# Optimization experiments

Hardware: AMD Instinct MI355X
Metric: run time of the kernel (lower is better)

## Reference

```python
import jax, jax.numpy as jnp
import numpy as np

B, H, S, D = 2, 16, 2048, 64
NUM_BUCKETS = 32
MAX_DISTANCE = 256


def setup_inputs() -> dict:
    key = jax.random.key(0)
    kq, kk, kv, kb, kl = jax.random.split(key, 5)
    q = jax.random.normal(kq, (B, H, S, D), dtype=jnp.float32)
    k = jax.random.normal(kk, (B, H, S, D), dtype=jnp.float32)
    v = jax.random.normal(kv, (B, H, S, D), dtype=jnp.float32)
    bias_table = jax.random.normal(kb, (NUM_BUCKETS, H), dtype=jnp.float32)
    event_length = jax.random.randint(kl, (B,), 1, S + 1, dtype=jnp.int64)
    return {"q": q, "k": k, "v": v, "bias_table": bias_table, "event_length": event_length}


def _relative_position_bucket(relative_position):
    # T5-style bucketing exactly as the torch module: n = -rel_pos
    half = NUM_BUCKETS // 2  # 16
    n = -relative_position
    is_small = n < half
    # guard log for the branch not taken (n<=0); where() masks it out
    nf = jnp.maximum(n, 1).astype(jnp.float32)
    val_if_large = half + jnp.minimum(
        jnp.log(nf / half) / np.log(MAX_DISTANCE / half) * (NUM_BUCKETS - half),
        NUM_BUCKETS - 1 - half,
    ).astype(jnp.int32)
    ret = jnp.where(is_small, n, val_if_large)
    return jnp.clip(ret, 0, NUM_BUCKETS - 1)


def _compute_bias(bias_table, seq_len):
    ctx = jnp.arange(seq_len)[:, None]
    mem = jnp.arange(seq_len)[None, :]
    rp_bucket = _relative_position_bucket(mem - ctx)  # (S,S)
    values = bias_table[rp_bucket]                    # (S,S,H)
    return jnp.transpose(values, (2, 0, 1))[None]     # (1,H,S,S)


def reference(q, k, v, bias_table, event_length):
    seq_len = q.shape[2]
    head_dim = q.shape[3]
    # scaled QK^T: (B,H,S,S)
    logits = jnp.einsum("bhsd,bhtd->bhst", q, k) / np.sqrt(head_dim).astype(np.float32)
    logits = logits + _compute_bias(bias_table, seq_len)
    # key-side padding mask from per-event lengths
    mask = jnp.arange(seq_len)[None, None, None, :] < event_length[:, None, None, None]
    logits = jnp.where(mask, logits, jnp.float32(-1e9))
    attn = jax.nn.softmax(logits, axis=-1)
    # dropout p=0.01 omitted (eval-mode deterministic reference)
    return jnp.einsum("bhst,bhtd->bhsd", attn, v)
```

## Files before the change

kernel.cpp:

```cpp
#include <hip/hip_runtime.h>

#define B_ 2
#define H_ 16
#define S_ 2048
#define D_ 64
#define BQ 128
#define BK 64
#define NQB (S_ / BQ)
#define NKT (S_ / BK)
#define LDSH 64
#define NBUF 3
#define LOG2E 1.4426950408889634f
#define FIXM 10.0f

#if __has_builtin(__builtin_amdgcn_exp2f)
#define EXP2F(x) __builtin_amdgcn_exp2f(x)
#else
#define EXP2F(x) __expf((x) * 0.6931471805599453f)
#endif

typedef _Float16 half8 __attribute__((ext_vector_type(8)));
typedef _Float16 half4 __attribute__((ext_vector_type(4)));
typedef __fp16   fp16x2 __attribute__((ext_vector_type(2)));
typedef float floatx4 __attribute__((ext_vector_type(4)));

#define VT_OFF  24576
#define LUT_OFF 49152
#define OX_STR  66
#define LX_OFF  33792
#define SMEM_BYTES 50176

__global__ __launch_bounds__(512, 4)
void t5_attn_kernel(const float* __restrict__ qg_, const float* __restrict__ kg_,
                    const float* __restrict__ vg_, const float* __restrict__ bt,
                    const int* __restrict__ elen, float* __restrict__ outg_)
{
    __shared__ __align__(16) unsigned char smem[SMEM_BYTES];
    _Float16* KL = reinterpret_cast<_Float16*>(smem);
    _Float16* VT = reinterpret_cast<_Float16*>(smem + VT_OFF);
    float*   lut = reinterpret_cast<float*>(smem + LUT_OFF);

    const int tid  = threadIdx.x;
    const int wave = tid >> 6;
    const int lane = tid & 63;
    const int quad = lane >> 4;
    const int t16  = lane & 15;
    const int t8   = t16 & 7;
    const int wq   = wave >> 1;
    const int kh   = wave & 1;

    const int f    = blockIdx.x + NQB * (blockIdx.y + H_ * blockIdx.z);
    const int qblk = (f >> 3) & 15;
    const int bh   = (f & 7) | ((f >> 7) << 3);
    const int h    = bh & 15;
    const int b    = bh >> 4;

    if (tid < 256) {
        int n = tid;
        int bucket;
        if (n < 16) {
            bucket = n;
        } else {
            int vl = (int)(__log2f((float)n * 0.0625f) * 4.0f);
            bucket = 16 + (vl < 15 ? vl : 15);
        }
        lut[n] = bt[bucket * H_ + h] * LOG2E - FIXM;
    }
    const float sh_next = FIXM - bt[h] * LOG2E;
    const float sh_far  = FIXM - bt[31 * H_ + h] * LOG2E;

    const int len = (elen[1] == 0) ? elen[2 * b] : elen[b];
    const int ntiles = (len + BK - 1) >> 6;

    const size_t bhoff = ((size_t)b * H_ + h) * (size_t)(S_ * D_);
    const float* qptr = qg_ + bhoff;
    const float* kptr = kg_ + bhoff;
    const float* vptr = vg_ + bhoff;
    float*       optr = outg_ + bhoff;

    half8 qf[2][2];
    {
        const float qscale = 0.125f * LOG2E;
        #pragma unroll
        for (int rg = 0; rg < 2; ++rg) {
            const int row = qblk * BQ + wq * 32 + rg * 16 + t16;
            const float* qp = qptr + (size_t)row * D_ + quad * 8;
            #pragma unroll
            for (int c = 0; c < 2; ++c) {
                const float4* pq = reinterpret_cast<const float4*>(qp + c * 32);
                float4 x0 = pq[0], x1 = pq[1];
                half8 hv;
                hv[0] = (_Float16)(x0.x * qscale); hv[1] = (_Float16)(x0.y * qscale);
                hv[2] = (_Float16)(x0.z * qscale); hv[3] = (_Float16)(x0.w * qscale);
                hv[4] = (_Float16)(x1.x * qscale); hv[5] = (_Float16)(x1.y * qscale);
                hv[6] = (_Float16)(x1.z * qscale); hv[7] = (_Float16)(x1.w * qscale);
                qf[rg][c] = hv;
            }
        }
    }

    floatx4 acc[2][4];
    float l_[2];
    #pragma unroll
    for (int rg = 0; rg < 2; ++rg) {
        #pragma unroll
        for (int nb = 0; nb < 4; ++nb) acc[rg][nb] = floatx4{0.f, 0.f, 0.f, 0.f};
        l_[rg] = 0.f;
    }

    const int i_lo = qblk * BQ + wq * 32;

    auto pack4 = [](const floatx4& v) -> half4 {
        fp16x2 lo = __builtin_amdgcn_cvt_pkrtz(v[0], v[1]);
        fp16x2 hi = __builtin_amdgcn_cvt_pkrtz(v[2], v[3]);
        half4 w;
        w[0] = (_Float16)lo[0]; w[1] = (_Float16)lo[1];
        w[2] = (_Float16)hi[0]; w[3] = (_Float16)hi[1];
        return w;
    };

    const int krow = tid >> 3;
    const int kst  = krow * LDSH + (((tid & 7) ^ (krow & 7)) << 3);
    const int vst  = lane * LDSH + ((wave ^ (lane & 7)) << 3);
    const int c8w  = (tid & 7) << 3;

    float4 kx0, kx1;
    float  vx[8];
    auto prefetch = [&](int kt) {
        const int ktc = kt < NKT ? kt : NKT - 1;
        const float4* pp = reinterpret_cast<const float4*>(
            kptr + (size_t)(ktc * BK + krow) * D_ + c8w);
        kx0 = pp[0];
        kx1 = pp[1];
        const float* vb = vptr + (size_t)(ktc * BK + wave * 8) * D_ + lane;
        #pragma unroll
        for (int jj = 0; jj < 8; ++jj)
            vx[jj] = vb[jj * D_];
    };
    auto stage = [&](int bufe) {
        half8 hv;
        hv[0]=(_Float16)kx0.x; hv[1]=(_Float16)kx0.y; hv[2]=(_Float16)kx0.z; hv[3]=(_Float16)kx0.w;
        hv[4]=(_Float16)kx1.x; hv[5]=(_Float16)kx1.y; hv[6]=(_Float16)kx1.z; hv[7]=(_Float16)kx1.w;
        *reinterpret_cast<half8*>(KL + bufe + kst) = hv;
        half8 vv;
        #pragma unroll
        for (int jj = 0; jj < 8; ++jj) vv[jj] = (_Float16)vx[jj];
        *reinterpret_cast<half8*>(VT + bufe + vst) = vv;
    };

    prefetch(0);
    stage(0);
    prefetch(1);
    __syncthreads();

    int cur = 0;
    for (int kt = 0; kt < ntiles; ++kt) {
        const int nxt  = (cur + 1 == NBUF) ? 0 : cur + 1;
        const int curb = cur * 4096;
        const int nxtb = nxt * 4096;

        stage(nxtb);
        prefetch(kt + 2);

        const int keybase = kt * BK + kh * 32;

        const bool unif_next = (i_lo + 31 <= keybase);
        const bool unif_far  = (i_lo >= keybase + 247);
        const float cinit = unif_next ? -sh_next : (unif_far ? -sh_far : 0.f);
        const floatx4 ci = {cinit, cinit, cinit, cinit};

        floatx4 sa[2][2];
        #pragma unroll
        for (int rg = 0; rg < 2; ++rg)
            #pragma unroll
            for (int nb = 0; nb < 2; ++nb) sa[rg][nb] = ci;
        __builtin_amdgcn_s_setprio(1);
        #pragma unroll
        for (int kc = 0; kc < 2; ++kc) {
            #pragma unroll
            for (int nb = 0; nb < 2; ++nb) {
                half8 af = *reinterpret_cast<const half8*>(
                    KL + curb + (kh * 32 + nb * 16 + t16) * LDSH +
                    ((((kc << 2) | quad) ^ t8) << 3));
                sa[0][nb] = __builtin_amdgcn_mfma_f32_16x16x32_f16(af, qf[0][kc], sa[0][nb], 0, 0, 0);
                sa[1][nb] = __builtin_amdgcn_mfma_f32_16x16x32_f16(af, qf[1][kc], sa[1][nb], 0, 0, 0);
            }
        }
        __builtin_amdgcn_s_setprio(0);

        half4 bvv[4][2];
        #pragma unroll
        for (int nb = 0; nb < 4; ++nb) {
            #pragma unroll
            for (int s = 0; s < 2; ++s) {
                bvv[nb][s] = *reinterpret_cast<const half4*>(
                    VT + curb + (nb * 16 + t16) * LDSH +
                    ((((kh << 2) | (s << 1) | (quad >> 1)) ^ t8) << 3) +
                    ((quad & 1) << 2));
            }
        }

        if (!unif_next && !unif_far) {
            #pragma unroll
            for (int rg = 0; rg < 2; ++rg) {
                const int d0 = i_lo + rg * 16 + t16 - keybase - quad * 4;
                #pragma unroll
                for (int nb = 0; nb < 2; ++nb) {
                    #pragma unroll
                    for (int r = 0; r < 4; ++r) {
                        int d = d0 - nb * 16 - r;
                        d = d < 0 ? 0 : (d > 255 ? 255 : d);
                        sa[rg][nb][r] += lut[d];
                    }
                }
            }
        }
        if ((kt == ntiles - 1) && (len & 63)) {
            #pragma unroll
            for (int nb = 0; nb < 2; ++nb) {
                #pragma unroll
                for (int r = 0; r < 4; ++r) {
                    bool valid = (keybase + nb * 16 + quad * 4 + r) < len;
                    #pragma unroll
                    for (int rg = 0; rg < 2; ++rg)
                        sa[rg][nb][r] = valid ? sa[rg][nb][r] : -1e30f;
                }
            }
        }

        #pragma unroll
        for (int rg = 0; rg < 2; ++rg) {
            float ssum = 0.f;
            #pragma unroll
            for (int nb = 0; nb < 2; ++nb)
                #pragma unroll
                for (int r = 0; r < 4; ++r) {
                    sa[rg][nb][r] = EXP2F(sa[rg][nb][r]);
                    ssum += sa[rg][nb][r];
                }
            l_[rg] += ssum;
        }

        {
            half4 aA0 = pack4(sa[0][0]);
            half4 aB0 = pack4(sa[0][1]);
            half4 aA1 = pack4(sa[1][0]);
            half4 aB1 = pack4(sa[1][1]);
            __builtin_amdgcn_s_setprio(1);
            #pragma unroll
            for (int nb = 0; nb < 4; ++nb) {
                acc[0][nb] = __builtin_amdgcn_mfma_f32_16x16x16f16(aA0, bvv[nb][0], acc[0][nb], 0, 0, 0);
                acc[0][nb] = __builtin_amdgcn_mfma_f32_16x16x16f16(aB0, bvv[nb][1], acc[0][nb], 0, 0, 0);
                acc[1][nb] = __builtin_amdgcn_mfma_f32_16x16x16f16(aA1, bvv[nb][0], acc[1][nb], 0, 0, 0);
                acc[1][nb] = __builtin_amdgcn_mfma_f32_16x16x16f16(aB1, bvv[nb][1], acc[1][nb], 0, 0, 0);
            }
            __builtin_amdgcn_s_setprio(0);
        }

        __syncthreads();
        cur = nxt;
    }

    float lh[2];
    #pragma unroll
    for (int rg = 0; rg < 2; ++rg) {
        float lv = l_[rg];
        lv += __shfl_xor(lv, 16, 64);
        lv += __shfl_xor(lv, 32, 64);
        lh[rg] = lv;
    }
    float* Ox = reinterpret_cast<float*>(smem);
    float* Lx = reinterpret_cast<float*>(smem + LX_OFF);
    if (kh == 1) {
        #pragma unroll
        for (int rg = 0; rg < 2; ++rg) {
            #pragma unroll
            for (int nb = 0; nb < 4; ++nb)
                #pragma unroll
                for (int r = 0; r < 4; ++r)
                    Ox[(wq * 32 + rg * 16 + quad * 4 + r) * OX_STR + nb * 16 + t16] =
                        acc[rg][nb][r];
            if (quad == 0) Lx[wq * 32 + rg * 16 + t16] = lh[rg];
        }
    }
    __syncthreads();
    if (kh == 0) {
        #pragma unroll
        for (int rg = 0; rg < 2; ++rg) {
            const float inv = 1.f / (lh[rg] + Lx[wq * 32 + rg * 16 + t16]);
            #pragma unroll
            for (int r = 0; r < 4; ++r) {
                const int rowloc = quad * 4 + r;
                const float invr = __shfl(inv, (lane & 48) | rowloc, 64);
                const int row = qblk * BQ + wq * 32 + rg * 16 + rowloc;
                #pragma unroll
                for (int nb = 0; nb < 4; ++nb)
                    optr[(size_t)row * D_ + nb * 16 + t16] =
                        (acc[rg][nb][r] +
                         Ox[(wq * 32 + rg * 16 + rowloc) * OX_STR + nb * 16 + t16]) * invr;
            }
        }
    }
}

extern "C" void kernel_launch(void* const* d_in, const int* in_sizes, int n_in,
                              void* d_out, int out_size, void* d_ws, size_t ws_size,
                              hipStream_t stream) {
    const float* q  = (const float*)d_in[0];
    const float* k  = (const float*)d_in[1];
    const float* v  = (const float*)d_in[2];
    const float* bt = (const float*)d_in[3];
    const int*   el = (const int*)d_in[4];
    float* out = (float*)d_out;
    dim3 grid(NQB, H_, B_);
    t5_attn_kernel<<<grid, 512, 0, stream>>>(q, k, v, bt, el, out);
}
```

Measured before the change: 123.3 us.

## Split keys of the longer batch across two blocks and combine partials

Adds a split-K path. Blocks for the batch with the longer event length are divided into two key-range halves, each writing unnormalized partial outputs and row sums to workspace, and a second combine kernel sums and normalizes them. The shorter batch runs whole in the first 256 blocks. This is meant to even out the load imbalance between the two batches. The change also shrinks the K/V LDS ring from triple to double buffering, with staging after compute, which lowers LDS use but may expose more load latency. It costs an extra kernel launch and a workspace round-trip.

```diff
diff --git a/kernel.cpp b/kernel.cpp
--- a/kernel.cpp
+++ b/kernel.cpp
@@ -9,7 +9,6 @@
 #define NQB (S_ / BQ)
 #define NKT (S_ / BK)
 #define LDSH 64
-#define NBUF 3
 #define LOG2E 1.4426950408889634f
 #define FIXM 10.0f
 
@@ -24,16 +23,21 @@
 typedef __fp16   fp16x2 __attribute__((ext_vector_type(2)));
 typedef float floatx4 __attribute__((ext_vector_type(4)));
 
-#define VT_OFF  24576
-#define LUT_OFF 49152
+#define VT_OFF  16384
+#define LUT_OFF 32768
 #define OX_STR  66
 #define LX_OFF  33792
-#define SMEM_BYTES 50176
-
+#define SMEM_BYTES 34304
+
+#define SLOT_F  8320
+#define WS_NEED (1024u + 512u * SLOT_F * 4u)
+
+template <bool SPLIT>
 __global__ __launch_bounds__(512, 4)
-void t5_attn_kernel(const float* __restrict__ qg_, const float* __restrict__ kg_,
-                    const float* __restrict__ vg_, const float* __restrict__ bt,
-                    const int* __restrict__ elen, float* __restrict__ outg_)
+void t5_attn(const float* __restrict__ qg_, const float* __restrict__ kg_,
+             const float* __restrict__ vg_, const float* __restrict__ bt,
+             const int* __restrict__ elen, float* __restrict__ outg_,
+             float* __restrict__ ws)
 {
     __shared__ __align__(16) unsigned char smem[SMEM_BYTES];
     _Float16* KL = reinterpret_cast<_Float16*>(smem);
@@ -45,15 +49,48 @@
     const int lane = tid & 63;
     const int quad = lane >> 4;
     const int t16  = lane & 15;
-    const int t8   = t16 & 7;
+    const int t8   = t16 & 15 & 7;
     const int wq   = wave >> 1;
     const int kh   = wave & 1;
 
-    const int f    = blockIdx.x + NQB * (blockIdx.y + H_ * blockIdx.z);
-    const int qblk = (f >> 3) & 15;
-    const int bh   = (f & 7) | ((f >> 7) << 3);
-    const int h    = bh & 15;
-    const int b    = bh >> 4;
+    int b, h, qblk, kt0, kt1, len;
+    bool partial = false;
+    int slotidx = 0;
+    if constexpr (!SPLIT) {
+        const int f = blockIdx.x + NQB * (blockIdx.y + H_ * blockIdx.z);
+        qblk = (f >> 3) & 15;
+        const int bh = (f & 7) | ((f >> 7) << 3);
+        h = bh & 15;
+        b = bh >> 4;
+        len = (elen[1] == 0) ? elen[2 * b] : elen[b];
+        kt0 = 0;
+        kt1 = (len + 63) >> 6;
+    } else {
+        const int f = blockIdx.x;
+        const int p = f & 255;
+        h    = (p & 7) | (((p >> 7) & 1) << 3);
+        qblk = (p >> 3) & 15;
+        const int l0 = elen[0];
+        const int l1 = (elen[1] == 0) ? elen[2] : elen[1];
+        const int lb_ = (l1 >= l0) ? 1 : 0;
+        if (f < 256) {
+            b   = 1 - lb_;
+            len = lb_ ? l0 : l1;
+            kt0 = 0;
+            kt1 = (len + 63) >> 6;
+        } else {
+            b   = lb_;
+            len = lb_ ? l1 : l0;
+            const int nt   = (len + 63) >> 6;
+            const int hh   = (nt + 1) >> 1;
+            const int part = (f >> 9) & 1;
+            kt0 = part ? hh : 0;
+            kt1 = part ? nt : hh;
+            partial = true;
+            slotidx = p * 2 + part;
+        }
+    }
+    const int ntb = (len + 63) >> 6;
 
     if (tid < 256) {
         int n = tid;
@@ -68,9 +105,6 @@
     }
     const float sh_next = FIXM - bt[h] * LOG2E;
     const float sh_far  = FIXM - bt[31 * H_ + h] * LOG2E;
-
-    const int len = (elen[1] == 0) ? elen[2 * b] : elen[b];
-    const int ntiles = (len + BK - 1) >> 6;
 
     const size_t bhoff = ((size_t)b * H_ + h) * (size_t)(S_ * D_);
     const float* qptr = qg_ + bhoff;
@@ -148,117 +182,117 @@
         *reinterpret_cast<half8*>(VT + bufe + vst) = vv;
     };
 
-    prefetch(0);
-    stage(0);
-    prefetch(1);
-    __syncthreads();
-
-    int cur = 0;
-    for (int kt = 0; kt < ntiles; ++kt) {
-        const int nxt  = (cur + 1 == NBUF) ? 0 : cur + 1;
-        const int curb = cur * 4096;
-        const int nxtb = nxt * 4096;
-
-        stage(nxtb);
-        prefetch(kt + 2);
-
-        const int keybase = kt * BK + kh * 32;
-
-        const bool unif_next = (i_lo + 31 <= keybase);
-        const bool unif_far  = (i_lo >= keybase + 247);
-        const float cinit = unif_next ? -sh_next : (unif_far ? -sh_far : 0.f);
-        const floatx4 ci = {cinit, cinit, cinit, cinit};
-
-        floatx4 sa[2][2];
-        #pragma unroll
-        for (int rg = 0; rg < 2; ++rg)
-            #pragma unroll
-            for (int nb = 0; nb < 2; ++nb) sa[rg][nb] = ci;
-        __builtin_amdgcn_s_setprio(1);
-        #pragma unroll
-        for (int kc = 0; kc < 2; ++kc) {
-            #pragma unroll
-            for (int nb = 0; nb < 2; ++nb) {
-                half8 af = *reinterpret_cast<const half8*>(
-                    KL + curb + (kh * 32 + nb * 16 + t16) * LDSH +
-                    ((((kc << 2) | quad) ^ t8) << 3));
-                sa[0][nb] = __builtin_amdgcn_mfma_f32_16x16x32_f16(af, qf[0][kc], sa[0][nb], 0, 0, 0);
-                sa[1][nb] = __builtin_amdgcn_mfma_f32_16x16x32_f16(af, qf[1][kc], sa[1][nb], 0, 0, 0);
-            }
-        }
-        __builtin_amdgcn_s_setprio(0);
-
-        half4 bvv[4][2];
-        #pragma unroll
-        for (int nb = 0; nb < 4; ++nb) {
-            #pragma unroll
-            for (int s = 0; s < 2; ++s) {
-                bvv[nb][s] = *reinterpret_cast<const half4*>(
-                    VT + curb + (nb * 16 + t16) * LDSH +
-                    ((((kh << 2) | (s << 1) | (quad >> 1)) ^ t8) << 3) +
-                    ((quad & 1) << 2));
-            }
-        }
-
-        if (!unif_next && !unif_far) {
-            #pragma unroll
-            for (int rg = 0; rg < 2; ++rg) {
-                const int d0 = i_lo + rg * 16 + t16 - keybase - quad * 4;
+    if (kt0 < kt1) {
+        prefetch(kt0);
+        stage(0);
+        __syncthreads();
+
+        for (int kt = kt0; kt < kt1; ++kt) {
+            const int cur  = (kt - kt0) & 1;
+            const int curb = cur * 4096;
+            const bool more = (kt + 1) < kt1;
+            if (more) prefetch(kt + 1);
+
+            const int keybase = kt * BK + kh * 32;
+
+            const bool unif_next = (i_lo + 31 <= keybase);
+            const bool unif_far  = (i_lo >= keybase + 247);
+            const float cinit = unif_next ? -sh_next : (unif_far ? -sh_far : 0.f);
+            const floatx4 ci = {cinit, cinit, cinit, cinit};
+
+            floatx4 sa[2][2];
+            #pragma unroll
+            for (int rg = 0; rg < 2; ++rg)
+                #pragma unroll
+                for (int nb = 0; nb < 2; ++nb) sa[rg][nb] = ci;
+            __builtin_amdgcn_s_setprio(1);
+            #pragma unroll
+            for (int kc = 0; kc < 2; ++kc) {
+                #pragma unroll
+                for (int nb = 0; nb < 2; ++nb) {
+                    half8 af = *reinterpret_cast<const half8*>(
+                        KL + curb + (kh * 32 + nb * 16 + t16) * LDSH +
+                        ((((kc << 2) | quad) ^ t8) << 3));
+                    sa[0][nb] = __builtin_amdgcn_mfma_f32_16x16x32_f16(af, qf[0][kc], sa[0][nb], 0, 0, 0);
+                    sa[1][nb] = __builtin_amdgcn_mfma_f32_16x16x32_f16(af, qf[1][kc], sa[1][nb], 0, 0, 0);
+                }
+            }
+            __builtin_amdgcn_s_setprio(0);
+
+            half4 bvv[4][2];
+            #pragma unroll
+            for (int nb = 0; nb < 4; ++nb) {
+                #pragma unroll
+                for (int s = 0; s < 2; ++s) {
+                    bvv[nb][s] = *reinterpret_cast<const half4*>(
+                        VT + curb + (nb * 16 + t16) * LDSH +
+                        ((((kh << 2) | (s << 1) | (quad >> 1)) ^ t8) << 3) +
+                        ((quad & 1) << 2));
+                }
+            }
+
+            if (!unif_next && !unif_far) {
+                #pragma unroll
+                for (int rg = 0; rg < 2; ++rg) {
+                    const int d0 = i_lo + rg * 16 + t16 - keybase - quad * 4;
+                    #pragma unroll
+                    for (int nb = 0; nb < 2; ++nb) {
+                        #pragma unroll
+                        for (int r = 0; r < 4; ++r) {
+                            int d = d0 - nb * 16 - r;
+                            d = d < 0 ? 0 : (d > 255 ? 255 : d);
+                            sa[rg][nb][r] += lut[d];
+                        }
+                    }
+                }
+            }
+            if ((kt == ntb - 1) && (len & 63)) {
                 #pragma unroll
                 for (int nb = 0; nb < 2; ++nb) {
                     #pragma unroll
                     for (int r = 0; r < 4; ++r) {
-                        int d = d0 - nb * 16 - r;
-                        d = d < 0 ? 0 : (d > 255 ? 255 : d);
-                        sa[rg][nb][r] += lut[d];
+                        bool valid = (keybase + nb * 16 + quad * 4 + r) < len;
+                        #pragma unroll
+                        for (int rg = 0; rg < 2; ++rg)
+                            sa[rg][nb][r] = valid ? sa[rg][nb][r] : -1e30f;
                     }
                 }
             }
-        }
-        if ((kt == ntiles - 1) && (len & 63)) {
-            #pragma unroll
-            for (int nb = 0; nb < 2; ++nb) {
-                #pragma unroll
-                for (int r = 0; r < 4; ++r) {
-                    bool valid = (keybase + nb * 16 + quad * 4 + r) < len;
+
+            #pragma unroll
+            for (int rg = 0; rg < 2; ++rg) {
+                float ssum = 0.f;
+                #pragma unroll
+                for (int nb = 0; nb < 2; ++nb)
                     #pragma unroll
-                    for (int rg = 0; rg < 2; ++rg)
-                        sa[rg][nb][r] = valid ? sa[rg][nb][r] : -1e30f;
-                }
-            }
-        }
-
-        #pragma unroll
-        for (int rg = 0; rg < 2; ++rg) {
-            float ssum = 0.f;
-            #pragma unroll
-            for (int nb = 0; nb < 2; ++nb)
-                #pragma unroll
-                for (int r = 0; r < 4; ++r) {
-                    sa[rg][nb][r] = EXP2F(sa[rg][nb][r]);
-                    ssum += sa[rg][nb][r];
-                }
-            l_[rg] += ssum;
-        }
-
-        {
-            half4 aA0 = pack4(sa[0][0]);
-            half4 aB0 = pack4(sa[0][1]);
-            half4 aA1 = pack4(sa[1][0]);
-            half4 aB1 = pack4(sa[1][1]);
-            __builtin_amdgcn_s_setprio(1);
-            #pragma unroll
-            for (int nb = 0; nb < 4; ++nb) {
-                acc[0][nb] = __builtin_amdgcn_mfma_f32_16x16x16f16(aA0, bvv[nb][0], acc[0][nb], 0, 0, 0);
-                acc[0][nb] = __builtin_amdgcn_mfma_f32_16x16x16f16(aB0, bvv[nb][1], acc[0][nb], 0, 0, 0);
-                acc[1][nb] = __builtin_amdgcn_mfma_f32_16x16x16f16(aA1, bvv[nb][0], acc[1][nb], 0, 0, 0);
-                acc[1][nb] = __builtin_amdgcn_mfma_f32_16x16x16f16(aB1, bvv[nb][1], acc[1][nb], 0, 0, 0);
-            }
-            __builtin_amdgcn_s_setprio(0);
-        }
-
+                    for (int r = 0; r < 4; ++r) {
+                        sa[rg][nb][r] = EXP2F(sa[rg][nb][r]);
+                        ssum += sa[rg][nb][r];
+                    }
+                l_[rg] += ssum;
+            }
+
+            {
+                half4 aA0 = pack4(sa[0][0]);
+                half4 aB0 = pack4(sa[0][1]);
+                half4 aA1 = pack4(sa[1][0]);
+                half4 aB1 = pack4(sa[1][1]);
+                __builtin_amdgcn_s_setprio(1);
+                #pragma unroll
+                for (int nb = 0; nb < 4; ++nb) {
+                    acc[0][nb] = __builtin_amdgcn_mfma_f32_16x16x16f16(aA0, bvv[nb][0], acc[0][nb], 0, 0, 0);
+                    acc[0][nb] = __builtin_amdgcn_mfma_f32_16x16x16f16(aB0, bvv[nb][1], acc[0][nb], 0, 0, 0);
+                    acc[1][nb] = __builtin_amdgcn_mfma_f32_16x16x16f16(aA1, bvv[nb][0], acc[1][nb], 0, 0, 0);
+                    acc[1][nb] = __builtin_amdgcn_mfma_f32_16x16x16f16(aB1, bvv[nb][1], acc[1][nb], 0, 0, 0);
+                }
+                __builtin_amdgcn_s_setprio(0);
+            }
+
+            if (more) stage((cur ^ 1) * 4096);
+            __syncthreads();
+        }
+    } else {
         __syncthreads();
-        cur = nxt;
     }
 
     float lh[2];
@@ -284,22 +318,75 @@
         }
     }
     __syncthreads();
-    if (kh == 0) {
-        #pragma unroll
-        for (int rg = 0; rg < 2; ++rg) {
-            const float inv = 1.f / (lh[rg] + Lx[wq * 32 + rg * 16 + t16]);
-            #pragma unroll
-            for (int r = 0; r < 4; ++r) {
-                const int rowloc = quad * 4 + r;
-                const float invr = __shfl(inv, (lane & 48) | rowloc, 64);
-                const int row = qblk * BQ + wq * 32 + rg * 16 + rowloc;
-                #pragma unroll
-                for (int nb = 0; nb < 4; ++nb)
-                    optr[(size_t)row * D_ + nb * 16 + t16] =
-                        (acc[rg][nb][r] +
-                         Ox[(wq * 32 + rg * 16 + rowloc) * OX_STR + nb * 16 + t16]) * invr;
-            }
-        }
+    if (!partial) {
+        if (kh == 0) {
+            #pragma unroll
+            for (int rg = 0; rg < 2; ++rg) {
+                const float inv = 1.f / (lh[rg] + Lx[wq * 32 + rg * 16 + t16]);
+                #pragma unroll
+                for (int r = 0; r < 4; ++r) {
+                    const int rowloc = quad * 4 + r;
+                    const float invr = __shfl(inv, (lane & 48) | rowloc, 64);
+                    const int row = qblk * BQ + wq * 32 + rg * 16 + rowloc;
+                    #pragma unroll
+                    for (int nb = 0; nb < 4; ++nb)
+                        optr[(size_t)row * D_ + nb * 16 + t16] =
+                            (acc[rg][nb][r] +
+                             Ox[(wq * 32 + rg * 16 + rowloc) * OX_STR + nb * 16 + t16]) * invr;
+                }
+            }
+        }
+    } else {
+        float* slot = ws + 256 + (size_t)slotidx * SLOT_F;
+        if (kh == 0) {
+            #pragma unroll
+            for (int rg = 0; rg < 2; ++rg) {
+                #pragma unroll
+                for (int r = 0; r < 4; ++r) {
+                    const int rloc = wq * 32 + rg * 16 + quad * 4 + r;
+                    #pragma unroll
+                    for (int nb = 0; nb < 4; ++nb)
+                        slot[rloc * D_ + nb * 16 + t16] =
+                            acc[rg][nb][r] + Ox[rloc * OX_STR + nb * 16 + t16];
+                }
+                if (quad == 0)
+                    slot[8192 + wq * 32 + rg * 16 + t16] =
+                        lh[rg] + Lx[wq * 32 + rg * 16 + t16];
+            }
+        }
+    }
+}
+
+__global__ __launch_bounds__(256)
+void t5_combine(const int* __restrict__ elen, const float* __restrict__ ws,
+                float* __restrict__ outg_)
+{
+    const int l0 = elen[0];
+    const int l1 = (elen[1] == 0) ? elen[2] : elen[1];
+    const int lb_ = (l1 >= l0) ? 1 : 0;
+
+    const int p    = blockIdx.x;
+    const int h    = (p & 7) | (((p >> 7) & 1) << 3);
+    const int qblk = (p >> 3) & 15;
+
+    const float* sA = ws + 256 + (size_t)(p * 2 + 0) * SLOT_F;
+    const float* sB = ws + 256 + (size_t)(p * 2 + 1) * SLOT_F;
+
+    const int row = threadIdx.x >> 1;
+    const int c32 = (threadIdx.x & 1) << 5;
+
+    const float inv = 1.f / (sA[8192 + row] + sB[8192 + row]);
+    const float* a  = sA + row * D_ + c32;
+    const float* bq = sB + row * D_ + c32;
+    float* od = outg_ + (((size_t)lb_ * H_ + h) * S_ + qblk * BQ + row) * D_ + c32;
+    #pragma unroll
+    for (int j = 0; j < 8; ++j) {
+        float4 x = *reinterpret_cast<const float4*>(a + j * 4);
+        float4 y = *reinterpret_cast<const float4*>(bq + j * 4);
+        float4 o;
+        o.x = (x.x + y.x) * inv; o.y = (x.y + y.y) * inv;
+        o.z = (x.z + y.z) * inv; o.w = (x.w + y.w) * inv;
+        *reinterpret_cast<float4*>(od + j * 4) = o;
     }
 }
 
@@ -312,6 +399,12 @@
     const float* bt = (const float*)d_in[3];
     const int*   el = (const int*)d_in[4];
     float* out = (float*)d_out;
-    dim3 grid(NQB, H_, B_);
-    t5_attn_kernel<<<grid, 512, 0, stream>>>(q, k, v, bt, el, out);
+    if (d_ws != nullptr && ws_size >= (size_t)WS_NEED) {
+        t5_attn<true><<<dim3(768), 512, 0, stream>>>(q, k, v, bt, el, out,
+                                                     (float*)d_ws);
+        t5_combine<<<dim3(256), 256, 0, stream>>>(el, (const float*)d_ws, out);
+    } else {
+        t5_attn<false><<<dim3(NQB, H_, B_), 512, 0, stream>>>(q, k, v, bt, el,
+                                                              out, nullptr);
+    }
 }
```

New measurement: 156.9 us. 1.27x slower.

## Pre-convert K/V to fp16 in workspace and stream tiles via global_load_lds

Applied to the files above, without the earlier changes.

Adds a prep kernel that converts K to fp16 and V to a transposed fp16 layout in the workspace. The attention kernel then loads tiles straight from global into LDS with global_load_lds, double-buffered, which removes per-block fp32 loads and register-side conversion. LDS use drops from three buffers to two, which may allow more blocks per CU. The cost is an extra kernel launch plus a full pass over K/V, and the direct-to-LDS path gives up the XOR swizzle, so LDS bank conflicts may rise. A fallback kernel runs when no workspace is provided.

```diff
diff --git a/kernel.cpp b/kernel.cpp
--- a/kernel.cpp
+++ b/kernel.cpp
@@ -9,7 +9,6 @@
 #define NQB (S_ / BQ)
 #define NKT (S_ / BK)
 #define LDSH 64
-#define NBUF 3
 #define LOG2E 1.4426950408889634f
 #define FIXM 10.0f
 
@@ -19,21 +18,78 @@
 #define EXP2F(x) __expf((x) * 0.6931471805599453f)
 #endif
 
+#if __has_builtin(__builtin_amdgcn_global_load_lds)
+#define HAS_GLDS 1
+#else
+#define HAS_GLDS 0
+#endif
+
 typedef _Float16 half8 __attribute__((ext_vector_type(8)));
 typedef _Float16 half4 __attribute__((ext_vector_type(4)));
 typedef __fp16   fp16x2 __attribute__((ext_vector_type(2)));
 typedef float floatx4 __attribute__((ext_vector_type(4)));
 
-#define VT_OFF  24576
-#define LUT_OFF 49152
+#define VT_OFF  16384
+#define LUT_OFF 32768
 #define OX_STR  66
 #define LX_OFF  33792
-#define SMEM_BYTES 50176
-
+#define SMEM_BYTES 34304
+
+#define KV_ELEMS (B_ * H_ * S_ * D_)
+#define WS_NEED  ((size_t)KV_ELEMS * 2 * 2)
+
+__global__ __launch_bounds__(256)
+void t5_prep(const float* __restrict__ kg_, const float* __restrict__ vg_,
+             _Float16* __restrict__ kws, _Float16* __restrict__ vws)
+{
+    const int t = threadIdx.x;
+    if (blockIdx.x < 1024) {
+        const float4* src = reinterpret_cast<const float4*>(kg_);
+        half4* dst = reinterpret_cast<half4*>(kws);
+        #pragma unroll
+        for (int it = 0; it < 4; ++it) {
+            const size_t i = (size_t)blockIdx.x * 1024 + it * 256 + t;
+            float4 x = src[i];
+            half4 hv;
+            hv[0] = (_Float16)x.x; hv[1] = (_Float16)x.y;
+            hv[2] = (_Float16)x.z; hv[3] = (_Float16)x.w;
+            dst[i] = hv;
+        }
+    } else {
+        __shared__ float vt[64][65];
+        const int tt = blockIdx.x - 1024;
+        const int bh = tt >> 5;
+        const int kt = tt & 31;
+        const float* vsrc = vg_ + (size_t)bh * (S_ * D_) + (size_t)kt * 64 * D_;
+        #pragma unroll
+        for (int it = 0; it < 4; ++it) {
+            const int idx = it * 256 + t;
+            const int key = idx >> 4;
+            const int c4  = (idx & 15) << 2;
+            float4 x = *reinterpret_cast<const float4*>(vsrc + key * D_ + c4);
+            vt[key][c4 + 0] = x.x; vt[key][c4 + 1] = x.y;
+            vt[key][c4 + 2] = x.z; vt[key][c4 + 3] = x.w;
+        }
+        __syncthreads();
+        const int d  = t >> 2;
+        const int kq = (t & 3) << 4;
+        half8 o0, o1;
+        #pragma unroll
+        for (int j = 0; j < 8; ++j) {
+            o0[j] = (_Float16)vt[kq + j][d];
+            o1[j] = (_Float16)vt[kq + 8 + j][d];
+        }
+        _Float16* dst = vws + (size_t)bh * (D_ * S_) + (size_t)d * S_ + kt * 64 + kq;
+        *reinterpret_cast<half8*>(dst)     = o0;
+        *reinterpret_cast<half8*>(dst + 8) = o1;
+    }
+}
+
+#if HAS_GLDS
 __global__ __launch_bounds__(512, 4)
-void t5_attn_kernel(const float* __restrict__ qg_, const float* __restrict__ kg_,
-                    const float* __restrict__ vg_, const float* __restrict__ bt,
-                    const int* __restrict__ elen, float* __restrict__ outg_)
+void t5_attn_g(const float* __restrict__ qg_, const _Float16* __restrict__ kws,
+               const _Float16* __restrict__ vws, const float* __restrict__ bt,
+               const int* __restrict__ elen, float* __restrict__ outg_)
 {
     __shared__ __align__(16) unsigned char smem[SMEM_BYTES];
     _Float16* KL = reinterpret_cast<_Float16*>(smem);
@@ -45,7 +101,6 @@
     const int lane = tid & 63;
     const int quad = lane >> 4;
     const int t16  = lane & 15;
-    const int t8   = t16 & 7;
     const int wq   = wave >> 1;
     const int kh   = wave & 1;
 
@@ -72,11 +127,11 @@
     const int len = (elen[1] == 0) ? elen[2 * b] : elen[b];
     const int ntiles = (len + BK - 1) >> 6;
 
-    const size_t bhoff = ((size_t)b * H_ + h) * (size_t)(S_ * D_);
-    const float* qptr = qg_ + bhoff;
-    const float* kptr = kg_ + bhoff;
-    const float* vptr = vg_ + bhoff;
-    float*       optr = outg_ + bhoff;
+    const size_t bho = ((size_t)b * H_ + h) * (size_t)(S_ * D_);
+    const float* qptr = qg_ + bho;
+    float*       optr = outg_ + bho;
+    const _Float16* kbh = kws + bho;
+    const _Float16* vbh = vws + ((size_t)b * H_ + h) * (size_t)(D_ * S_);
 
     half8 qf[2][2];
     {
@@ -119,6 +174,254 @@
         return w;
     };
 
+    const int lrow = lane >> 3;
+    const int lchk = (lane & 7) << 3;
+    const _Float16* ksrc = kbh + (wave * 8 + lrow) * D_ + lchk;
+    const _Float16* vsrc = vbh + (size_t)(wave * 8 + lrow) * S_ + lchk;
+    const int dstoff = wave * 512;
+
+    auto issue = [&](int kt, int bufe) {
+        __builtin_amdgcn_global_load_lds(
+            (const __attribute__((address_space(1))) void*)(ksrc + (size_t)kt * 4096),
+            (__attribute__((address_space(3))) void*)(KL + bufe + dstoff), 16, 0, 0);
+        __builtin_amdgcn_global_load_lds(
+            (const __attribute__((address_space(1))) void*)(vsrc + (size_t)kt * 64),
+            (__attribute__((address_space(3))) void*)(VT + bufe + dstoff), 16, 0, 0);
+    };
+
+    issue(0, 0);
+    __syncthreads();
+
+    for (int kt = 0; kt < ntiles; ++kt) {
+        const int curb = (kt & 1) * 4096;
+        if (kt + 1 < ntiles) issue(kt + 1, curb ^ 4096);
+
+        const int keybase = kt * BK + kh * 32;
+
+        const bool unif_next = (i_lo + 31 <= keybase);
+        const bool unif_far  = (i_lo >= keybase + 247);
+        const float cinit = unif_next ? -sh_next : (unif_far ? -sh_far : 0.f);
+        const floatx4 ci = {cinit, cinit, cinit, cinit};
+
+        floatx4 sa[2][2];
+        #pragma unroll
+        for (int rg = 0; rg < 2; ++rg)
+            #pragma unroll
+            for (int nb = 0; nb < 2; ++nb) sa[rg][nb] = ci;
+        __builtin_amdgcn_s_setprio(1);
+        #pragma unroll
+        for (int kc = 0; kc < 2; ++kc) {
+            #pragma unroll
+            for (int nb = 0; nb < 2; ++nb) {
+                half8 af = *reinterpret_cast<const half8*>(
+                    KL + curb + (kh * 32 + nb * 16 + t16) * LDSH + kc * 32 + quad * 8);
+                sa[0][nb] = __builtin_amdgcn_mfma_f32_16x16x32_f16(af, qf[0][kc], sa[0][nb], 0, 0, 0);
+                sa[1][nb] = __builtin_amdgcn_mfma_f32_16x16x32_f16(af, qf[1][kc], sa[1][nb], 0, 0, 0);
+            }
+        }
+        __builtin_amdgcn_s_setprio(0);
+
+        half4 bvv[4][2];
+        #pragma unroll
+        for (int nb = 0; nb < 4; ++nb) {
+            #pragma unroll
+            for (int s = 0; s < 2; ++s) {
+                bvv[nb][s] = *reinterpret_cast<const half4*>(
+                    VT + curb + (nb * 16 + t16) * LDSH + kh * 32 + s * 16 + quad * 4);
+            }
+        }
+
+        if (!unif_next && !unif_far) {
+            #pragma unroll
+            for (int rg = 0; rg < 2; ++rg) {
+                const int d0 = i_lo + rg * 16 + t16 - keybase - quad * 4;
+                #pragma unroll
+                for (int nb = 0; nb < 2; ++nb) {
+                    #pragma unroll
+                    for (int r = 0; r < 4; ++r) {
+                        int d = d0 - nb * 16 - r;
+                        d = d < 0 ? 0 : (d > 255 ? 255 : d);
+                        sa[rg][nb][r] += lut[d];
+                    }
+                }
+            }
+        }
+        if ((kt == ntiles - 1) && (len & 63)) {
+            #pragma unroll
+            for (int nb = 0; nb < 2; ++nb) {
+                #pragma unroll
+                for (int r = 0; r < 4; ++r) {
+                    bool valid = (keybase + nb * 16 + quad * 4 + r) < len;
+                    #pragma unroll
+                    for (int rg = 0; rg < 2; ++rg)
+                        sa[rg][nb][r] = valid ? sa[rg][nb][r] : -1e30f;
+                }
+            }
+        }
+
+        #pragma unroll
+        for (int rg = 0; rg < 2; ++rg) {
+            float ssum = 0.f;
+            #pragma unroll
+            for (int nb = 0; nb < 2; ++nb)
+                #pragma unroll
+                for (int r = 0; r < 4; ++r) {
+                    sa[rg][nb][r] = EXP2F(sa[rg][nb][r]);
+                    ssum += sa[rg][nb][r];
+                }
+            l_[rg] += ssum;
+        }
+
+        {
+            half4 aA0 = pack4(sa[0][0]);
+            half4 aB0 = pack4(sa[0][1]);
+            half4 aA1 = pack4(sa[1][0]);
+            half4 aB1 = pack4(sa[1][1]);
+            __builtin_amdgcn_s_setprio(1);
+            #pragma unroll
+            for (int nb = 0; nb < 4; ++nb) {
+                acc[0][nb] = __builtin_amdgcn_mfma_f32_16x16x16f16(aA0, bvv[nb][0], acc[0][nb], 0, 0, 0);
+                acc[0][nb] = __builtin_amdgcn_mfma_f32_16x16x16f16(aB0, bvv[nb][1], acc[0][nb], 0, 0, 0);
+                acc[1][nb] = __builtin_amdgcn_mfma_f32_16x16x16f16(aA1, bvv[nb][0], acc[1][nb], 0, 0, 0);
+                acc[1][nb] = __builtin_amdgcn_mfma_f32_16x16x16f16(aB1, bvv[nb][1], acc[1][nb], 0, 0, 0);
+            }
+            __builtin_amdgcn_s_setprio(0);
+        }
+
+        __syncthreads();
+    }
+
+    float lh[2];
+    #pragma unroll
+    for (int rg = 0; rg < 2; ++rg) {
+        float lv = l_[rg];
+        lv += __shfl_xor(lv, 16, 64);
+        lv += __shfl_xor(lv, 32, 64);
+        lh[rg] = lv;
+    }
+    float* Ox = reinterpret_cast<float*>(smem);
+    float* Lx = reinterpret_cast<float*>(smem + LX_OFF);
+    if (kh == 1) {
+        #pragma unroll
+        for (int rg = 0; rg < 2; ++rg) {
+            #pragma unroll
+            for (int nb = 0; nb < 4; ++nb)
+                #pragma unroll
+                for (int r = 0; r < 4; ++r)
+                    Ox[(wq * 32 + rg * 16 + quad * 4 + r) * OX_STR + nb * 16 + t16] =
+                        acc[rg][nb][r];
+            if (quad == 0) Lx[wq * 32 + rg * 16 + t16] = lh[rg];
+        }
+    }
+    __syncthreads();
+    if (kh == 0) {
+        #pragma unroll
+        for (int rg = 0; rg < 2; ++rg) {
+            const float inv = 1.f / (lh[rg] + Lx[wq * 32 + rg * 16 + t16]);
+            #pragma unroll
+            for (int r = 0; r < 4; ++r) {
+                const int rowloc = quad * 4 + r;
+                const float invr = __shfl(inv, (lane & 48) | rowloc, 64);
+                const int row = qblk * BQ + wq * 32 + rg * 16 + rowloc;
+                #pragma unroll
+                for (int nb = 0; nb < 4; ++nb)
+                    optr[(size_t)row * D_ + nb * 16 + t16] =
+                        (acc[rg][nb][r] +
+                         Ox[(wq * 32 + rg * 16 + rowloc) * OX_STR + nb * 16 + t16]) * invr;
+            }
+        }
+    }
+}
+#endif
+
+__global__ __launch_bounds__(512, 4)
+void t5_attn_fb(const float* __restrict__ qg_, const float* __restrict__ kg_,
+                const float* __restrict__ vg_, const float* __restrict__ bt,
+                const int* __restrict__ elen, float* __restrict__ outg_)
+{
+    __shared__ __align__(16) unsigned char smem[SMEM_BYTES];
+    _Float16* KL = reinterpret_cast<_Float16*>(smem);
+    _Float16* VT = reinterpret_cast<_Float16*>(smem + VT_OFF);
+    float*   lut = reinterpret_cast<float*>(smem + LUT_OFF);
+
+    const int tid  = threadIdx.x;
+    const int wave = tid >> 6;
+    const int lane = tid & 63;
+    const int quad = lane >> 4;
+    const int t16  = lane & 15;
+    const int t8   = t16 & 7;
+    const int wq   = wave >> 1;
+    const int kh   = wave & 1;
+
+    const int f    = blockIdx.x + NQB * (blockIdx.y + H_ * blockIdx.z);
+    const int qblk = (f >> 3) & 15;
+    const int bh   = (f & 7) | ((f >> 7) << 3);
+    const int h    = bh & 15;
+    const int b    = bh >> 4;
+
+    if (tid < 256) {
+        int n = tid;
+        int bucket;
+        if (n < 16) bucket = n;
+        else {
+            int vl = (int)(__log2f((float)n * 0.0625f) * 4.0f);
+            bucket = 16 + (vl < 15 ? vl : 15);
+        }
+        lut[n] = bt[bucket * H_ + h] * LOG2E - FIXM;
+    }
+    const float sh_next = FIXM - bt[h] * LOG2E;
+    const float sh_far  = FIXM - bt[31 * H_ + h] * LOG2E;
+
+    const int len = (elen[1] == 0) ? elen[2 * b] : elen[b];
+    const int ntiles = (len + BK - 1) >> 6;
+
+    const size_t bhoff = ((size_t)b * H_ + h) * (size_t)(S_ * D_);
+    const float* qptr = qg_ + bhoff;
+    const float* kptr = kg_ + bhoff;
+    const float* vptr = vg_ + bhoff;
+    float*       optr = outg_ + bhoff;
+
+    half8 qf[2][2];
+    {
+        const float qscale = 0.125f * LOG2E;
+        #pragma unroll
+        for (int rg = 0; rg < 2; ++rg) {
+            const int row = qblk * BQ + wq * 32 + rg * 16 + t16;
+            const float* qp = qptr + (size_t)row * D_ + quad * 8;
+            #pragma unroll
+            for (int c = 0; c < 2; ++c) {
+                const float4* pq = reinterpret_cast<const float4*>(qp + c * 32);
+                float4 x0 = pq[0], x1 = pq[1];
+                half8 hv;
+                hv[0] = (_Float16)(x0.x * qscale); hv[1] = (_Float16)(x0.y * qscale);
+                hv[2] = (_Float16)(x0.z * qscale); hv[3] = (_Float16)(x0.w * qscale);
+                hv[4] = (_Float16)(x1.x * qscale); hv[5] = (_Float16)(x1.y * qscale);
+                hv[6] = (_Float16)(x1.z * qscale); hv[7] = (_Float16)(x1.w * qscale);
+                qf[rg][c] = hv;
+            }
+        }
+    }
+
+    floatx4 acc[2][4];
+    float l_[2];
+    #pragma unroll
+    for (int rg = 0; rg < 2; ++rg) {
+        #pragma unroll
+        for (int nb = 0; nb < 4; ++nb) acc[rg][nb] = floatx4{0.f, 0.f, 0.f, 0.f};
+        l_[rg] = 0.f;
+    }
+
+    const int i_lo = qblk * BQ + wq * 32;
+
+    auto pack4 = [](const floatx4& v) -> half4 {
+        fp16x2 lo = __builtin_amdgcn_cvt_pkrtz(v[0], v[1]);
+        fp16x2 hi = __builtin_amdgcn_cvt_pkrtz(v[2], v[3]);
+        half4 w;
+        w[0] = (_Float16)lo[0]; w[1] = (_Float16)lo[1];
+        w[2] = (_Float16)hi[0]; w[3] = (_Float16)hi[1];
+        return w;
+    };
+
     const int krow = tid >> 3;
     const int kst  = krow * LDSH + (((tid & 7) ^ (krow & 7)) << 3);
     const int vst  = lane * LDSH + ((wave ^ (lane & 7)) << 3);
@@ -150,20 +453,14 @@
 
     prefetch(0);
     stage(0);
-    prefetch(1);
     __syncthreads();
 
-    int cur = 0;
     for (int kt = 0; kt < ntiles; ++kt) {
-        const int nxt  = (cur + 1 == NBUF) ? 0 : cur + 1;
-        const int curb = cur * 4096;
-        const int nxtb = nxt * 4096;
-
-        stage(nxtb);
-        prefetch(kt + 2);
+        const int curb = (kt & 1) * 4096;
+        const bool more = (kt + 1) < ntiles;
+        if (more) prefetch(kt + 1);
 
         const int keybase = kt * BK + kh * 32;
-
         const bool unif_next = (i_lo + 31 <= keybase);
         const bool unif_far  = (i_lo >= keybase + 247);
         const float cinit = unif_next ? -sh_next : (unif_far ? -sh_far : 0.f);
@@ -257,8 +554,8 @@
             __builtin_amdgcn_s_setprio(0);
         }
 
+        if (more) stage(curb ^ 4096);
         __syncthreads();
-        cur = nxt;
     }
 
     float lh[2];
@@ -312,6 +609,14 @@
     const float* bt = (const float*)d_in[3];
     const int*   el = (const int*)d_in[4];
     float* out = (float*)d_out;
-    dim3 grid(NQB, H_, B_);
-    t5_attn_kernel<<<grid, 512, 0, stream>>>(q, k, v, bt, el, out);
+#if HAS_GLDS
+    if (d_ws != nullptr && ws_size >= WS_NEED) {
+        _Float16* kws = (_Float16*)d_ws;
+        _Float16* vws = kws + KV_ELEMS;
+        t5_prep<<<dim3(2048), 256, 0, stream>>>(k, v, kws, vws);
+        t5_attn_g<<<dim3(NQB, H_, B_), 512, 0, stream>>>(q, kws, vws, bt, el, out);
+        return;
+    }
+#endif
+    t5_attn_fb<<<dim3(NQB, H_, B_), 512, 0, stream>>>(q, k, v, bt, el, out);
 }
```

After: 124.0 us. No clear change (+0.5%).
